# Performance work log

Measured on AMD Instinct MI355X. Metric: run time of the kernel, lower is better.

The kernel has to match this reference:

```python
import jax, jax.numpy as jnp
import numpy as np

# static config (matches init_kwargs and a standard 4-level FPN for ~800px input)
SPATIAL_SHAPES = ((100, 100), (50, 50), (25, 25), (13, 13))  # (H_l, W_l)
B, C, H, L, P = 2, 256, 8, 4, 4
DFFN = 2048
DH = C // H
LQ = sum(h * w for h, w in SPATIAL_SHAPES)  # 13294


def layer_norm(x, g, b, eps=1e-5):
    m = jnp.mean(x, -1, keepdims=True)
    v = jnp.mean((x - m) ** 2, -1, keepdims=True)
    return (x - m) * jax.lax.rsqrt(v + eps) * g + b


def ms_deform_sample(value, loc, attn):
    # value [B,Lv,H,DH], loc [B,Lq,H,L,P,2] in [0,1], attn [B,Lq,H,L,P]
    value = jnp.transpose(value, (0, 2, 1, 3))  # [B,H,Lv,DH]
    lq = loc.shape[1]
    out = jnp.zeros((B, H, lq, DH), value.dtype)
    start = 0
    for l, (Hl, Wl) in enumerate(SPATIAL_SHAPES):
        v = jax.lax.dynamic_slice_in_dim(value, start, Hl * Wl, axis=2)  # [B,H,N_l,DH]
        # grid_sample(align_corners=False) coords: x = loc_x*W - 0.5
        gx = jnp.transpose(loc[:, :, :, l, :, 0], (0, 2, 1, 3)) * Wl - 0.5  # [B,H,Lq,P]
        gy = jnp.transpose(loc[:, :, :, l, :, 1], (0, 2, 1, 3)) * Hl - 0.5
        aw = jnp.transpose(attn[:, :, :, l, :], (0, 2, 1, 3))  # [B,H,Lq,P]
        x0 = jnp.floor(gx)
        y0 = jnp.floor(gy)
        for dx in (0.0, 1.0):
            for dy in (0.0, 1.0):
                xi = x0 + dx
                yi = y0 + dy
                w = (1.0 - jnp.abs(gx - xi)) * (1.0 - jnp.abs(gy - yi))
                valid = (xi >= 0) & (xi < Wl) & (yi >= 0) & (yi < Hl)
                idx = (jnp.clip(yi, 0, Hl - 1) * Wl + jnp.clip(xi, 0, Wl - 1)).astype(jnp.int32)
                g = jnp.take_along_axis(v, idx.reshape(B, H, -1)[..., None], axis=2)  # [B,H,Lq*P,DH]
                ww = (w * aw * valid.astype(w.dtype))[..., None]  # [B,H,Lq,P,1]
                out = out + jnp.sum(g.reshape(B, H, lq, P, DH) * ww, axis=3)
        start += Hl * Wl
    return jnp.transpose(out, (0, 2, 1, 3)).reshape(B, lq, C)


def setup_inputs() -> dict:
    key = jax.random.key(0)
    ks = jax.random.split(key, 16)
    s = 0.02
    return {
        "src": jax.random.normal(ks[0], (B, LQ, C), jnp.float32),
        "pos": jax.random.normal(ks[1], (B, LQ, C), jnp.float32),
        "reference_points": jax.random.uniform(ks[2], (B, LQ, L, 2), jnp.float32),
        "w_value": jax.random.normal(ks[3], (C, C), jnp.float32) * s,
        "b_value": jnp.zeros((C,), jnp.float32),
        "w_off": jax.random.normal(ks[4], (C, H * L * P * 2), jnp.float32) * s,
        "b_off": jax.random.normal(ks[5], (H * L * P * 2,), jnp.float32) * s,
        "w_attn": jax.random.normal(ks[6], (C, H * L * P), jnp.float32) * s,
        "b_attn": jnp.zeros((H * L * P,), jnp.float32),
        "w_out": jax.random.normal(ks[7], (C, C), jnp.float32) * s,
        "b_out": jnp.zeros((C,), jnp.float32),
        "ln1_g": jnp.ones((C,), jnp.float32),
        "ln1_b": jnp.zeros((C,), jnp.float32),
        "w_ffn1": jax.random.normal(ks[8], (C, DFFN), jnp.float32) * s,
        "b_ffn1": jnp.zeros((DFFN,), jnp.float32),
        "w_ffn2": jax.random.normal(ks[9], (DFFN, C), jnp.float32) * s,
        "b_ffn2": jnp.zeros((C,), jnp.float32),
        "ln2_g": jnp.ones((C,), jnp.float32),
        "ln2_b": jnp.zeros((C,), jnp.float32),
    }


def reference(src, pos, reference_points, w_value, b_value, w_off, b_off, w_attn, b_attn,
              w_out, b_out, ln1_g, ln1_b, w_ffn1, b_ffn1, w_ffn2, b_ffn2, ln2_g, ln2_b):
    # DeformableTransformerEncoderLayer.forward (eval mode, no dropout)
    q = src + pos  # with_pos_embed
    lq = q.shape[1]
    value = (src @ w_value + b_value).reshape(B, -1, H, DH)
    off = (q @ w_off + b_off).reshape(B, lq, H, L, P, 2)
    attn = (q @ w_attn + b_attn).reshape(B, lq, H, L * P)
    attn = jax.nn.softmax(attn, axis=-1).reshape(B, lq, H, L, P)
    # offset_normalizer = (W_l, H_l)
    norm = jnp.array([[w, h] for h, w in SPATIAL_SHAPES], dtype=src.dtype)
    loc = reference_points[:, :, None, :, None, :] + off / norm[None, None, None, :, None, :]
    src2 = ms_deform_sample(value, loc, attn) @ w_out + b_out
    x = layer_norm(src + src2, ln1_g, ln1_b)
    ff = jax.nn.relu(x @ w_ffn1 + b_ffn1) @ w_ffn2 + b_ffn2
    return layer_norm(x + ff, ln2_g, ln2_b)
```

## Files before the change

kernel.cpp:

```cpp
#include <hip/hip_runtime.h>

#define LQN   13294
#define NBAT  2
#define MROWS (NBAT * LQN)
#define CCH   256
#define NHEAD 8
#define DHEAD 32
#define NLVL  4
#define NPT   4
#define DFF   2048

typedef short short8 __attribute__((ext_vector_type(8)));
typedef float f32x4 __attribute__((ext_vector_type(4)));
typedef unsigned short u16;
typedef u16 u16x4 __attribute__((ext_vector_type(4)));

__device__ __forceinline__ u16 f2bf(float f) {
  unsigned int u = __builtin_bit_cast(unsigned int, f);
  u += 0x7fffu + ((u >> 16) & 1u);
  return (u16)(u >> 16);
}
__device__ __forceinline__ float bf2f(u16 s) {
  unsigned int u = ((unsigned int)s) << 16;
  return __builtin_bit_cast(float, u);
}
__device__ __forceinline__ void async16(const void* g, void* l) {
  __builtin_amdgcn_global_load_lds(
      (const __attribute__((address_space(1))) void*)g,
      (__attribute__((address_space(3))) void*)l, 16, 0, 0);
}

template<int OUT_MODE>
__global__ __launch_bounds__(256, 2)
void gemm_bf16(const u16* __restrict__ A, const u16* __restrict__ BT,
               const float* __restrict__ bias, void* __restrict__ Cout,
               int M, int N, int K)
{
  __shared__ u16 As[2][128 * 64];
  __shared__ u16 Bs[2][128 * 64];
  const int t    = threadIdx.x;
  const int lane = t & 63;
  const int wid  = t >> 6;
  const int wm   = wid >> 1, wn = wid & 1;
  const int bm   = blockIdx.x, bn = blockIdx.y;
  const int l15  = lane & 15;
  const int kq   = lane >> 4;

  f32x4 acc[4][4];
#pragma unroll
  for (int m = 0; m < 4; ++m)
#pragma unroll
    for (int n = 0; n < 4; ++n) acc[m][n] = (f32x4)0.0f;

  auto stage = [&](int buf, int kt) {
#pragma unroll
    for (int i = 0; i < 4; ++i) {
      const int c   = i * 256 + t;
      const int row = c >> 3;
      const int kg  = (c & 7) ^ (row & 7);
      int ar = bm * 128 + row; ar = ar < M ? ar : M - 1;
      async16(&A[(size_t)ar * K + kt + kg * 8], &As[buf][c * 8]);
      const int br = bn * 128 + row;
      async16(&BT[(size_t)br * K + kt + kg * 8], &Bs[buf][c * 8]);
    }
  };

  stage(0, 0);
  __syncthreads();
  int cur = 0;

  for (int kt = 0; kt < K; kt += 64) {
    if (kt + 64 < K) stage(cur ^ 1, kt + 64);

#pragma unroll
    for (int kk = 0; kk < 2; ++kk) {
      short8 af[4], bfr[4];
#pragma unroll
      for (int m = 0; m < 4; ++m) {
        const int row = wm * 64 + m * 16 + l15;
        const int xb  = (kk * 64 + kq * 16) ^ ((row & 7) << 4);
        af[m] = *(const short8*)((const char*)&As[cur][0] + row * 128 + xb);
      }
#pragma unroll
      for (int n = 0; n < 4; ++n) {
        const int col = wn * 64 + n * 16 + l15;
        const int xb  = (kk * 64 + kq * 16) ^ ((col & 7) << 4);
        bfr[n] = *(const short8*)((const char*)&Bs[cur][0] + col * 128 + xb);
      }
#pragma unroll
      for (int m = 0; m < 4; ++m)
#pragma unroll
        for (int n = 0; n < 4; ++n)
          acc[m][n] = __builtin_amdgcn_mfma_f32_16x16x32_bf16(af[m], bfr[n], acc[m][n], 0, 0, 0);
    }

    __syncthreads();
    cur ^= 1;
  }

  const int crow0 = bm * 128 + wm * 64;
  const int ccol0 = bn * 128 + wn * 64;
#pragma unroll
  for (int n = 0; n < 4; ++n) {
    int col = ccol0 + n * 16 + l15;
    float bv = bias[col];
#pragma unroll
    for (int m = 0; m < 4; ++m) {
      int rbase = crow0 + m * 16 + kq * 4;
#pragma unroll
      for (int j = 0; j < 4; ++j) {
        int row = rbase + j;
        if (row < M) {
          float v = acc[m][n][j] + bv;
          if constexpr (OUT_MODE == 0) ((float*)Cout)[(size_t)row * N + col] = v;
          else                         ((u16*)Cout)[(size_t)row * N + col] = f2bf(v);
        }
      }
    }
  }
}

__global__ __launch_bounds__(256, 2)
void gemm_dual(const u16* __restrict__ A0, const u16* __restrict__ BT0,
               const float* __restrict__ bias0, u16* __restrict__ C0,
               const u16* __restrict__ A1, const u16* __restrict__ BT1,
               const float* __restrict__ bias1, float* __restrict__ C1)
{
  __shared__ u16 As[2][128 * 64];
  __shared__ u16 Bs[2][128 * 64];
  const int t    = threadIdx.x;
  const int lane = t & 63;
  const int wid  = t >> 6;
  const int wm   = wid >> 1, wn = wid & 1;
  const int bm   = blockIdx.x;
  const int bnG  = blockIdx.y;
  const bool first = bnG < 2;
  const u16* A    = first ? A0 : A1;
  const u16* BT   = first ? BT0 : BT1;
  const float* bias = first ? bias0 : bias1;
  const int  bn   = first ? bnG : bnG - 2;
  const int l15  = lane & 15;
  const int kq   = lane >> 4;

  f32x4 acc[4][4];
#pragma unroll
  for (int m = 0; m < 4; ++m)
#pragma unroll
    for (int n = 0; n < 4; ++n) acc[m][n] = (f32x4)0.0f;

  auto stage = [&](int buf, int kt) {
#pragma unroll
    for (int i = 0; i < 4; ++i) {
      const int c   = i * 256 + t;
      const int row = c >> 3;
      const int kg  = (c & 7) ^ (row & 7);
      int ar = bm * 128 + row; ar = ar < MROWS ? ar : MROWS - 1;
      async16(&A[(size_t)ar * 256 + kt + kg * 8], &As[buf][c * 8]);
      const int br = bn * 128 + row;
      async16(&BT[(size_t)br * 256 + kt + kg * 8], &Bs[buf][c * 8]);
    }
  };

  stage(0, 0);
  __syncthreads();
  int cur = 0;

  for (int kt = 0; kt < 256; kt += 64) {
    if (kt + 64 < 256) stage(cur ^ 1, kt + 64);

#pragma unroll
    for (int kk = 0; kk < 2; ++kk) {
      short8 af[4], bfr[4];
#pragma unroll
      for (int m = 0; m < 4; ++m) {
        const int row = wm * 64 + m * 16 + l15;
        const int xb  = (kk * 64 + kq * 16) ^ ((row & 7) << 4);
        af[m] = *(const short8*)((const char*)&As[cur][0] + row * 128 + xb);
      }
#pragma unroll
      for (int n = 0; n < 4; ++n) {
        const int col = wn * 64 + n * 16 + l15;
        const int xb  = (kk * 64 + kq * 16) ^ ((col & 7) << 4);
        bfr[n] = *(const short8*)((const char*)&Bs[cur][0] + col * 128 + xb);
      }
#pragma unroll
      for (int m = 0; m < 4; ++m)
#pragma unroll
        for (int n = 0; n < 4; ++n)
          acc[m][n] = __builtin_amdgcn_mfma_f32_16x16x32_bf16(af[m], bfr[n], acc[m][n], 0, 0, 0);
    }

    __syncthreads();
    cur ^= 1;
  }

  const int crow0 = bm * 128 + wm * 64;
  const int ccol0 = bn * 128 + wn * 64;
#pragma unroll
  for (int n = 0; n < 4; ++n) {
    int col = ccol0 + n * 16 + l15;
    float bv = bias[col];
#pragma unroll
    for (int m = 0; m < 4; ++m) {
      int rbase = crow0 + m * 16 + kq * 4;
#pragma unroll
      for (int j = 0; j < 4; ++j) {
        int row = rbase + j;
        if (row < MROWS) {
          float v = acc[m][n][j] + bv;
          if (first) C0[(size_t)row * 256 + col] = f2bf(v);
          else       C1[(size_t)row * 384 + col] = v;
        }
      }
    }
  }
}

__global__ __launch_bounds__(1024, 4)
void ffn_fused(const u16* __restrict__ x_bf, const u16* __restrict__ W1T,
               const u16* __restrict__ W2T, const float* __restrict__ b1,
               const float* __restrict__ b2, float* __restrict__ out)
{
  extern __shared__ char smem[];
  u16*  w1s = (u16*)(smem);
  u16*  w2s = (u16*)(smem + 65536);
  char* ps  = smem + 131072;

  const int t    = threadIdx.x;
  const int lane = t & 63;
  const int wid  = t >> 6;
  const int l15  = lane & 15;
  const int kq   = lane >> 4;
  const int bm   = blockIdx.x;
  const int pwm  = wid >> 1, pwn = wid & 1;
  const int vwm  = wid >> 2, vwn = wid & 3;

  short8 xr[8];
  {
    int ar = bm * 128 + pwm * 16 + l15;
    ar = ar < MROWS ? ar : MROWS - 1;
    const char* xb = (const char*)x_bf + (size_t)ar * 512 + kq * 16;
#pragma unroll
    for (int ks = 0; ks < 8; ++ks) xr[ks] = *(const short8*)(xb + ks * 64);
  }

  auto stage = [&](int buf, int it) {
#pragma unroll
    for (int i = 0; i < 2; ++i) {
      const int c  = i * 1024 + t;
      const int r1 = c >> 5;
      const int k1 = ((c & 31) ^ (r1 & 7)) * 8;
      async16(&W1T[(size_t)(it * 64 + r1) * 256 + k1], &w1s[buf * 16384 + c * 8]);
      const int r2 = c >> 3;
      const int k2 = ((c & 7) ^ (r2 & 7)) * 8;
      async16(&W2T[(size_t)r2 * 2048 + it * 64 + k2], &w2s[buf * 16384 + c * 8]);
    }
  };

  f32x4 acc[2][4];
#pragma unroll
  for (int m = 0; m < 2; ++m)
#pragma unroll
    for (int n = 0; n < 4; ++n) acc[m][n] = (f32x4)0.0f;

  stage(0, 0);
  __syncthreads();

  for (int it = 0; it < 32; ++it) {
    const int cur = it & 1;
    if (it < 31) stage(cur ^ 1, it + 1);

    f32x4 p[2];
    p[0] = (f32x4)0.0f; p[1] = (f32x4)0.0f;
#pragma unroll
    for (int ks = 0; ks < 8; ++ks) {
#pragma unroll
      for (int n = 0; n < 2; ++n) {
        const int wrow = pwn * 32 + n * 16 + l15;
        const int xb   = (((ks * 4 + kq) ^ (wrow & 7)) << 4);
        const short8 bfr = *(const short8*)((const char*)&w1s[cur * 16384] + wrow * 512 + xb);
        p[n] = __builtin_amdgcn_mfma_f32_16x16x32_bf16(xr[ks], bfr, p[n], 0, 0, 0);
      }
    }

#pragma unroll
    for (int n = 0; n < 2; ++n) {
      const int col = pwn * 32 + n * 16 + l15;
      const float bv = b1[it * 64 + col];
#pragma unroll
      for (int j = 0; j < 4; ++j) {
        const int prow = pwm * 16 + kq * 4 + j;
        *(u16*)(ps + prow * 144 + col * 2) = f2bf(fmaxf(p[n][j] + bv, 0.0f));
      }
    }
    __syncthreads();

#pragma unroll
    for (int kk = 0; kk < 2; ++kk) {
      short8 paf[2];
#pragma unroll
      for (int m = 0; m < 2; ++m) {
        const int arow = vwm * 32 + m * 16 + l15;
        paf[m] = *(const short8*)(ps + arow * 144 + (kk * 4 + kq) * 16);
      }
#pragma unroll
      for (int n = 0; n < 4; ++n) {
        const int brow = vwn * 64 + n * 16 + l15;
        const int xb   = (((kk * 4 + kq) ^ (brow & 7)) << 4);
        const short8 bfr = *(const short8*)((const char*)&w2s[cur * 16384] + brow * 128 + xb);
#pragma unroll
        for (int m = 0; m < 2; ++m)
          acc[m][n] = __builtin_amdgcn_mfma_f32_16x16x32_bf16(paf[m], bfr, acc[m][n], 0, 0, 0);
      }
    }
    __syncthreads();
  }

#pragma unroll
  for (int n = 0; n < 4; ++n) {
    const int col = vwn * 64 + n * 16 + l15;
    const float bv = b2[col];
#pragma unroll
    for (int m = 0; m < 2; ++m) {
      const int rbase = bm * 128 + vwm * 32 + m * 16 + kq * 4;
#pragma unroll
      for (int j = 0; j < 4; ++j) {
        const int row = rbase + j;
        if (row < MROWS) out[(size_t)row * 256 + col] = acc[m][n][j] + bv;
      }
    }
  }
}

__global__ __launch_bounds__(256)
void sampler_kernel(const float* __restrict__ offattn,
                    const float* __restrict__ refp,
                    const u16*  __restrict__ value,
                    u16*        __restrict__ src2)
{
  __shared__ float2 sWI[4][8][65];

  const int t    = threadIdx.x;
  const int r4   = t >> 6;
  const int lane = t & 63;
  const int row  = blockIdx.x * 4 + r4;
  const int b    = row / LQN;

  {
    const float* oa = offattn + (size_t)row * 384;
    const float* rp = refp + (size_t)row * 8;
    const int p16 = lane & 15;
    const int l   = p16 >> 2;
    const int Wl  = (l == 0) ? 100 : (l == 1) ? 50 : (l == 2) ? 25 : 13;
    const int st  = (l == 0) ? 0 : (l == 1) ? 10000 : (l == 2) ? 12500 : 13125;
    const float rx = rp[l * 2 + 0] * (float)Wl - 0.5f;
    const float ry = rp[l * 2 + 1] * (float)Wl - 0.5f;

#pragma unroll
    for (int s = 0; s < 2; ++s) {
      const int h = s * 4 + (lane >> 4);
      float logit = oa[256 + h * 16 + p16];
      float mx = logit;
#pragma unroll
      for (int o = 1; o < 16; o <<= 1) mx = fmaxf(mx, __shfl_xor(mx, o, 64));
      float e = __expf(logit - mx);
      float ssum = e;
#pragma unroll
      for (int o = 1; o < 16; o <<= 1) ssum += __shfl_xor(ssum, o, 64);
      const float aw = e / ssum;

      const float ox = oa[(h * 16 + p16) * 2 + 0];
      const float oy = oa[(h * 16 + p16) * 2 + 1];
      const float gx = rx + ox;
      const float gy = ry + oy;
      const float x0f = floorf(gx), y0f = floorf(gy);
      const int   x0 = (int)x0f, y0 = (int)y0f;
      const float fx = gx - x0f, fy = gy - y0f;
#pragma unroll
      for (int c = 0; c < 4; ++c) {
        const int dx = c & 1, dy = c >> 1;
        const int xi = x0 + dx, yi = y0 + dy;
        const float wx = dx ? fx : 1.0f - fx;
        const float wy = dy ? fy : 1.0f - fy;
        const bool valid = (xi >= 0) && (xi < Wl) && (yi >= 0) && (yi < Wl);
        const int xc = min(max(xi, 0), Wl - 1);
        const int yc = min(max(yi, 0), Wl - 1);
        const int idx = st + yc * Wl + xc;
        const float w = wx * wy * aw * (valid ? 1.0f : 0.0f);
        sWI[r4][h][p16 * 4 + c] = make_float2(w, __builtin_bit_cast(float, idx));
      }
    }
  }
  __syncthreads();

  {
    const int h  = lane >> 3;
    const int c4 = lane & 7;
    const char* vbase = (const char*)value + (size_t)b * LQN * 512 + h * 64 + c4 * 8;
    const float2* wi = sWI[r4][h];

    float a0 = 0.f, a1 = 0.f, a2 = 0.f, a3 = 0.f;
#pragma unroll 16
    for (int e = 0; e < 64; ++e) {
      const float2 p = wi[e];
      const float w  = p.x;
      const int  idx = __builtin_bit_cast(int, p.y);
      const unsigned long long u = *(const unsigned long long*)(vbase + (size_t)idx * 512);
      a0 += w * bf2f((u16)(u));
      a1 += w * bf2f((u16)(u >> 16));
      a2 += w * bf2f((u16)(u >> 32));
      a3 += w * bf2f((u16)(u >> 48));
    }
    u16x4 o;
    o[0] = f2bf(a0); o[1] = f2bf(a1); o[2] = f2bf(a2); o[3] = f2bf(a3);
    *(u16x4*)&src2[(size_t)row * 256 + h * 32 + c4 * 4] = o;
  }
}

template<int WRITE_BF>
__global__ __launch_bounds__(256)
void ln_kernel(const float* __restrict__ Xa, const float* __restrict__ Xb,
               const float* __restrict__ gam, const float* __restrict__ bet,
               float* __restrict__ Yf, u16* __restrict__ Ybf)
{
  const int wid = threadIdx.x >> 6, lane = threadIdx.x & 63;
  const int row = blockIdx.x * 4 + wid;
  const f32x4 va = ((const f32x4*)(Xa + (size_t)row * 256))[lane];
  const f32x4 vb = ((const f32x4*)(Xb + (size_t)row * 256))[lane];
  f32x4 v = va + vb;
  float s1 = v[0] + v[1] + v[2] + v[3];
  float s2 = v[0] * v[0] + v[1] * v[1] + v[2] * v[2] + v[3] * v[3];
#pragma unroll
  for (int off = 32; off; off >>= 1) {
    s1 += __shfl_xor(s1, off, 64);
    s2 += __shfl_xor(s2, off, 64);
  }
  const float mean = s1 * (1.0f / 256.0f);
  const float var  = s2 * (1.0f / 256.0f) - mean * mean;
  const float rstd = rsqrtf(var + 1e-5f);
  const f32x4 gv = ((const f32x4*)gam)[lane];
  const f32x4 bv = ((const f32x4*)bet)[lane];
  f32x4 y;
#pragma unroll
  for (int j = 0; j < 4; ++j) y[j] = (v[j] - mean) * rstd * gv[j] + bv[j];
  ((f32x4*)(Yf + (size_t)row * 256))[lane] = y;
  if constexpr (WRITE_BF) {
    u16x4 o;
#pragma unroll
    for (int j = 0; j < 4; ++j) o[j] = f2bf(y[j]);
    ((u16x4*)(Ybf + (size_t)row * 256))[lane] = o;
  }
}

__global__ __launch_bounds__(256)
void prep_qsrc(const float* __restrict__ src, const float* __restrict__ pos,
               u16* __restrict__ src_bf, u16* __restrict__ q_bf)
{
  const size_t i = (size_t)blockIdx.x * 256 + threadIdx.x;
  const f32x4 s = ((const f32x4*)src)[i];
  const f32x4 p = ((const f32x4*)pos)[i];
  u16x4 sb, qb;
#pragma unroll
  for (int j = 0; j < 4; ++j) { sb[j] = f2bf(s[j]); qb[j] = f2bf(s[j] + p[j]); }
  ((u16x4*)src_bf)[i] = sb;
  ((u16x4*)q_bf)[i]   = qb;
}

__global__ __launch_bounds__(256)
void prep_weights(const float* __restrict__ w_value, const float* __restrict__ w_off,
                  const float* __restrict__ w_attn,  const float* __restrict__ w_out,
                  const float* __restrict__ w_ffn1,  const float* __restrict__ w_ffn2,
                  const float* __restrict__ b_off,   const float* __restrict__ b_attn,
                  u16* __restrict__ WT_val, u16* __restrict__ WT_oa, u16* __restrict__ WT_out,
                  u16* __restrict__ WT_f1,  u16* __restrict__ WT_f2, float* __restrict__ bias_oa)
{
  int i = blockIdx.x * 256 + threadIdx.x;
  if (i < 65536) {
    const int k = i >> 8, n = i & 255;
    WT_val[n * 256 + k] = f2bf(w_value[i]);
  } else if ((i -= 65536) < 65536) {
    const int k = i >> 8, n = i & 255;
    WT_oa[n * 256 + k] = f2bf(w_off[i]);
  } else if ((i -= 65536) < 32768) {
    const int k = i >> 7, n = i & 127;
    WT_oa[(256 + n) * 256 + k] = f2bf(w_attn[i]);
  } else if ((i -= 32768) < 65536) {
    const int k = i >> 8, n = i & 255;
    WT_out[n * 256 + k] = f2bf(w_out[i]);
  } else if ((i -= 65536) < 524288) {
    const int k = i >> 11, n = i & 2047;
    WT_f1[n * 256 + k] = f2bf(w_ffn1[i]);
  } else if ((i -= 524288) < 524288) {
    const int k = i >> 8, n = i & 255;
    WT_f2[n * 2048 + k] = f2bf(w_ffn2[i]);
  } else if ((i -= 524288) < 384) {
    bias_oa[i] = (i < 256) ? b_off[i] : b_attn[i - 256];
  }
}

extern "C" void kernel_launch(void* const* d_in, const int* in_sizes, int n_in,
                              void* d_out, int out_size, void* d_ws, size_t ws_size,
                              hipStream_t stream)
{
  const float* src     = (const float*)d_in[0];
  const float* pos     = (const float*)d_in[1];
  const float* refp    = (const float*)d_in[2];
  const float* w_value = (const float*)d_in[3];
  const float* b_value = (const float*)d_in[4];
  const float* w_off   = (const float*)d_in[5];
  const float* b_off   = (const float*)d_in[6];
  const float* w_attn  = (const float*)d_in[7];
  const float* b_attn  = (const float*)d_in[8];
  const float* w_out   = (const float*)d_in[9];
  const float* b_out   = (const float*)d_in[10];
  const float* ln1_g   = (const float*)d_in[11];
  const float* ln1_b   = (const float*)d_in[12];
  const float* w_ffn1  = (const float*)d_in[13];
  const float* b_ffn1  = (const float*)d_in[14];
  const float* w_ffn2  = (const float*)d_in[15];
  const float* b_ffn2  = (const float*)d_in[16];
  const float* ln2_g   = (const float*)d_in[17];
  const float* ln2_b   = (const float*)d_in[18];

  char* ws = (char*)d_ws;
  size_t off = 0;
  auto alloc = [&](size_t bytes) { void* p = ws + off; off += (bytes + 255) & ~(size_t)255; return p; };

  u16*   src_bf   = (u16*)  alloc((size_t)MROWS * 256 * 2);
  u16*   q_bf     = (u16*)  alloc((size_t)MROWS * 256 * 2);
  float* offattn  = (float*)alloc((size_t)MROWS * 384 * 4);
  u16*   value_bf = (u16*)  alloc((size_t)MROWS * 256 * 2);
  u16*   src2_bf  = (u16*)  alloc((size_t)MROWS * 256 * 2);
  float* x_f32    = (float*)alloc((size_t)MROWS * 256 * 4);
  u16*   WT_val   = (u16*)  alloc(256 * 256 * 2);
  u16*   WT_oa    = (u16*)  alloc(384 * 256 * 2);
  u16*   WT_out   = (u16*)  alloc(256 * 256 * 2);
  u16*   WT_f1    = (u16*)  alloc(2048 * 256 * 2);
  u16*   WT_f2    = (u16*)  alloc((size_t)256 * 2048 * 2);
  float* bias_oa  = (float*)alloc(384 * 4);

  float* src2p = offattn;
  u16*   x_bf  = q_bf;
  float* ff    = (float*)value_bf;

  prep_weights<<<4994, 256, 0, stream>>>(w_value, w_off, w_attn, w_out, w_ffn1, w_ffn2,
                                         b_off, b_attn,
                                         WT_val, WT_oa, WT_out, WT_f1, WT_f2, bias_oa);

  prep_qsrc<<<6647, 256, 0, stream>>>(src, pos, src_bf, q_bf);

  static bool attr_set = false;
  if (!attr_set) {
    hipFuncSetAttribute((const void*)ffn_fused,
                        hipFuncAttributeMaxDynamicSharedMemorySize, 149504);
    attr_set = true;
  }

  gemm_dual<<<dim3(208, 5), 256, 0, stream>>>(src_bf, WT_val, b_value, value_bf,
                                              q_bf, WT_oa, bias_oa, offattn);

  sampler_kernel<<<MROWS / 4, 256, 0, stream>>>(offattn, refp, value_bf, src2_bf);

  gemm_bf16<0><<<dim3(208, 2), 256, 0, stream>>>(src2_bf, WT_out, b_out, src2p, MROWS, 256, 256);

  ln_kernel<1><<<6647, 256, 0, stream>>>(src, src2p, ln1_g, ln1_b, x_f32, x_bf);

  ffn_fused<<<208, 1024, 149504, stream>>>(x_bf, WT_f1, WT_f2, b_ffn1, b_ffn2, ff);

  ln_kernel<0><<<6647, 256, 0, stream>>>(x_f32, ff, ln2_g, ln2_b, (float*)d_out, nullptr);
}
```

Before: 252.7 us.

## Fuse residual and layernorm into the out-projection and FFN GEMM epilogues

```diff
diff --git a/kernel.cpp b/kernel.cpp
--- a/kernel.cpp
+++ b/kernel.cpp
@@ -28,96 +28,6 @@
   __builtin_amdgcn_global_load_lds(
       (const __attribute__((address_space(1))) void*)g,
       (__attribute__((address_space(3))) void*)l, 16, 0, 0);
-}
-
-template<int OUT_MODE>
-__global__ __launch_bounds__(256, 2)
-void gemm_bf16(const u16* __restrict__ A, const u16* __restrict__ BT,
-               const float* __restrict__ bias, void* __restrict__ Cout,
-               int M, int N, int K)
-{
-  __shared__ u16 As[2][128 * 64];
-  __shared__ u16 Bs[2][128 * 64];
-  const int t    = threadIdx.x;
-  const int lane = t & 63;
-  const int wid  = t >> 6;
-  const int wm   = wid >> 1, wn = wid & 1;
-  const int bm   = blockIdx.x, bn = blockIdx.y;
-  const int l15  = lane & 15;
-  const int kq   = lane >> 4;
-
-  f32x4 acc[4][4];
-#pragma unroll
-  for (int m = 0; m < 4; ++m)
-#pragma unroll
-    for (int n = 0; n < 4; ++n) acc[m][n] = (f32x4)0.0f;
-
-  auto stage = [&](int buf, int kt) {
-#pragma unroll
-    for (int i = 0; i < 4; ++i) {
-      const int c   = i * 256 + t;
-      const int row = c >> 3;
-      const int kg  = (c & 7) ^ (row & 7);
-      int ar = bm * 128 + row; ar = ar < M ? ar : M - 1;
-      async16(&A[(size_t)ar * K + kt + kg * 8], &As[buf][c * 8]);
-      const int br = bn * 128 + row;
-      async16(&BT[(size_t)br * K + kt + kg * 8], &Bs[buf][c * 8]);
-    }
-  };
-
-  stage(0, 0);
-  __syncthreads();
-  int cur = 0;
-
-  for (int kt = 0; kt < K; kt += 64) {
-    if (kt + 64 < K) stage(cur ^ 1, kt + 64);
-
-#pragma unroll
-    for (int kk = 0; kk < 2; ++kk) {
-      short8 af[4], bfr[4];
-#pragma unroll
-      for (int m = 0; m < 4; ++m) {
-        const int row = wm * 64 + m * 16 + l15;
-        const int xb  = (kk * 64 + kq * 16) ^ ((row & 7) << 4);
-        af[m] = *(const short8*)((const char*)&As[cur][0] + row * 128 + xb);
-      }
-#pragma unroll
-      for (int n = 0; n < 4; ++n) {
-        const int col = wn * 64 + n * 16 + l15;
-        const int xb  = (kk * 64 + kq * 16) ^ ((col & 7) << 4);
-        bfr[n] = *(const short8*)((const char*)&Bs[cur][0] + col * 128 + xb);
-      }
-#pragma unroll
-      for (int m = 0; m < 4; ++m)
-#pragma unroll
-        for (int n = 0; n < 4; ++n)
-          acc[m][n] = __builtin_amdgcn_mfma_f32_16x16x32_bf16(af[m], bfr[n], acc[m][n], 0, 0, 0);
-    }
-
-    __syncthreads();
-    cur ^= 1;
-  }
-
-  const int crow0 = bm * 128 + wm * 64;
-  const int ccol0 = bn * 128 + wn * 64;
-#pragma unroll
-  for (int n = 0; n < 4; ++n) {
-    int col = ccol0 + n * 16 + l15;
-    float bv = bias[col];
-#pragma unroll
-    for (int m = 0; m < 4; ++m) {
-      int rbase = crow0 + m * 16 + kq * 4;
-#pragma unroll
-      for (int j = 0; j < 4; ++j) {
-        int row = rbase + j;
-        if (row < M) {
-          float v = acc[m][n][j] + bv;
-          if constexpr (OUT_MODE == 0) ((float*)Cout)[(size_t)row * N + col] = v;
-          else                         ((u16*)Cout)[(size_t)row * N + col] = f2bf(v);
-        }
-      }
-    }
-  }
 }
 
 __global__ __launch_bounds__(256, 2)
@@ -216,15 +126,166 @@
   }
 }
 
-__global__ __launch_bounds__(1024, 4)
-void ffn_fused(const u16* __restrict__ x_bf, const u16* __restrict__ W1T,
-               const u16* __restrict__ W2T, const float* __restrict__ b1,
-               const float* __restrict__ b2, float* __restrict__ out)
+__global__ __launch_bounds__(512, 1)
+void outproj_ln1(const u16* __restrict__ src2_bf, const u16* __restrict__ WT_out,
+                 const float* __restrict__ b_out, const float* __restrict__ src,
+                 const float* __restrict__ g1, const float* __restrict__ be1,
+                 float* __restrict__ x_f32, u16* __restrict__ x_bf)
+{
+  extern __shared__ char smem[];
+  char* As0 = smem;
+  char* As1 = smem + 16384;
+  char* Bs0 = smem + 32768;
+  char* Bs1 = smem + 65536;
+  float2* red = (float2*)(smem + 98304);
+
+  const int t    = threadIdx.x;
+  const int lane = t & 63;
+  const int wid  = t >> 6;
+  const int wm   = wid >> 2, wn = wid & 3;
+  const int l15  = lane & 15;
+  const int kq   = lane >> 4;
+  const int bm   = blockIdx.x;
+
+  auto stage = [&](char* Abuf, char* Bbuf, int kt) {
+#pragma unroll
+    for (int i = 0; i < 2; ++i) {
+      const int c   = i * 512 + t;
+      const int row = c >> 3;
+      const int kg  = (c & 7) ^ (row & 7);
+      int ar = bm * 128 + row; ar = ar < MROWS ? ar : MROWS - 1;
+      async16(&src2_bf[(size_t)ar * 256 + kt + kg * 8], Abuf + c * 16);
+    }
+#pragma unroll
+    for (int i = 0; i < 4; ++i) {
+      const int c   = i * 512 + t;
+      const int row = c >> 3;
+      const int kg  = (c & 7) ^ (row & 7);
+      async16(&WT_out[(size_t)row * 256 + kt + kg * 8], Bbuf + c * 16);
+    }
+  };
+
+  f32x4 acc[4][4];
+#pragma unroll
+  for (int m = 0; m < 4; ++m)
+#pragma unroll
+    for (int n = 0; n < 4; ++n) acc[m][n] = (f32x4)0.0f;
+
+  stage(As0, Bs0, 0);
+  __syncthreads();
+
+  for (int kt = 0; kt < 256; kt += 64) {
+    const int cur = (kt >> 6) & 1;
+    char* Ause = cur ? As1 : As0;
+    char* Buse = cur ? Bs1 : Bs0;
+    if (kt + 64 < 256) stage(cur ? As0 : As1, cur ? Bs0 : Bs1, kt + 64);
+
+#pragma unroll
+    for (int kk = 0; kk < 2; ++kk) {
+      short8 af[4], bfr[4];
+#pragma unroll
+      for (int m = 0; m < 4; ++m) {
+        const int row = wm * 64 + m * 16 + l15;
+        const int xb  = (kk * 64 + kq * 16) ^ ((row & 7) << 4);
+        af[m] = *(const short8*)(Ause + row * 128 + xb);
+      }
+#pragma unroll
+      for (int n = 0; n < 4; ++n) {
+        const int col = wn * 64 + n * 16 + l15;
+        const int xb  = (kk * 64 + kq * 16) ^ ((col & 7) << 4);
+        bfr[n] = *(const short8*)(Buse + col * 128 + xb);
+      }
+#pragma unroll
+      for (int m = 0; m < 4; ++m)
+#pragma unroll
+        for (int n = 0; n < 4; ++n)
+          acc[m][n] = __builtin_amdgcn_mfma_f32_16x16x32_bf16(af[m], bfr[n], acc[m][n], 0, 0, 0);
+    }
+    __syncthreads();
+  }
+
+#pragma unroll
+  for (int n = 0; n < 4; ++n) {
+    const int col = wn * 64 + n * 16 + l15;
+    const float bv = b_out[col];
+#pragma unroll
+    for (int m = 0; m < 4; ++m)
+#pragma unroll
+      for (int j = 0; j < 4; ++j) {
+        int row = bm * 128 + wm * 64 + m * 16 + kq * 4 + j;
+        row = row < MROWS ? row : MROWS - 1;
+        acc[m][n][j] += bv + src[(size_t)row * 256 + col];
+      }
+  }
+  float s1[4][4], s2[4][4];
+#pragma unroll
+  for (int m = 0; m < 4; ++m)
+#pragma unroll
+    for (int j = 0; j < 4; ++j) {
+      float a = 0.f, b = 0.f;
+#pragma unroll
+      for (int n = 0; n < 4; ++n) { const float v = acc[m][n][j]; a += v; b += v * v; }
+      s1[m][j] = a; s2[m][j] = b;
+    }
+#pragma unroll
+  for (int o = 1; o < 16; o <<= 1)
+#pragma unroll
+    for (int m = 0; m < 4; ++m)
+#pragma unroll
+      for (int j = 0; j < 4; ++j) {
+        s1[m][j] += __shfl_xor(s1[m][j], o, 64);
+        s2[m][j] += __shfl_xor(s2[m][j], o, 64);
+      }
+  if (l15 == 0)
+#pragma unroll
+    for (int m = 0; m < 4; ++m)
+#pragma unroll
+      for (int j = 0; j < 4; ++j)
+        red[(wm * 64 + m * 16 + kq * 4 + j) * 4 + wn] = make_float2(s1[m][j], s2[m][j]);
+  __syncthreads();
+  float mean[4][4], rstd[4][4];
+#pragma unroll
+  for (int m = 0; m < 4; ++m)
+#pragma unroll
+    for (int j = 0; j < 4; ++j) {
+      const int rl = wm * 64 + m * 16 + kq * 4 + j;
+      float a = 0.f, b = 0.f;
+#pragma unroll
+      for (int w = 0; w < 4; ++w) { const float2 r = red[rl * 4 + w]; a += r.x; b += r.y; }
+      const float mu = a * (1.0f / 256.0f);
+      mean[m][j] = mu;
+      rstd[m][j] = rsqrtf(b * (1.0f / 256.0f) - mu * mu + 1e-5f);
+    }
+#pragma unroll
+  for (int n = 0; n < 4; ++n) {
+    const int col = wn * 64 + n * 16 + l15;
+    const float gg = g1[col], bb = be1[col];
+#pragma unroll
+    for (int m = 0; m < 4; ++m)
+#pragma unroll
+      for (int j = 0; j < 4; ++j) {
+        const int row = bm * 128 + wm * 64 + m * 16 + kq * 4 + j;
+        if (row < MROWS) {
+          const float y = (acc[m][n][j] - mean[m][j]) * rstd[m][j] * gg + bb;
+          x_f32[(size_t)row * 256 + col] = y;
+          x_bf[(size_t)row * 256 + col] = f2bf(y);
+        }
+      }
+  }
+}
+
+__global__ __launch_bounds__(1024, 2)
+void ffn_ln2(const u16* __restrict__ x_bf, const u16* __restrict__ W1T,
+             const u16* __restrict__ W2T, const float* __restrict__ b1,
+             const float* __restrict__ b2, const float* __restrict__ x_f32,
+             const float* __restrict__ g2, const float* __restrict__ be2,
+             float* __restrict__ out)
 {
   extern __shared__ char smem[];
   u16*  w1s = (u16*)(smem);
   u16*  w2s = (u16*)(smem + 65536);
   char* ps  = smem + 131072;
+  float2* red = (float2*)(smem + 149504);
 
   const int t    = threadIdx.x;
   const int lane = t & 63;
@@ -321,14 +382,65 @@
     const int col = vwn * 64 + n * 16 + l15;
     const float bv = b2[col];
 #pragma unroll
-    for (int m = 0; m < 2; ++m) {
-      const int rbase = bm * 128 + vwm * 32 + m * 16 + kq * 4;
-#pragma unroll
-      for (int j = 0; j < 4; ++j) {
-        const int row = rbase + j;
-        if (row < MROWS) out[(size_t)row * 256 + col] = acc[m][n][j] + bv;
-      }
-    }
+    for (int m = 0; m < 2; ++m)
+#pragma unroll
+      for (int j = 0; j < 4; ++j) {
+        int row = bm * 128 + vwm * 32 + m * 16 + kq * 4 + j;
+        row = row < MROWS ? row : MROWS - 1;
+        acc[m][n][j] += bv + x_f32[(size_t)row * 256 + col];
+      }
+  }
+  float s1[2][4], s2[2][4];
+#pragma unroll
+  for (int m = 0; m < 2; ++m)
+#pragma unroll
+    for (int j = 0; j < 4; ++j) {
+      float a = 0.f, b = 0.f;
+#pragma unroll
+      for (int n = 0; n < 4; ++n) { const float v = acc[m][n][j]; a += v; b += v * v; }
+      s1[m][j] = a; s2[m][j] = b;
+    }
+#pragma unroll
+  for (int o = 1; o < 16; o <<= 1)
+#pragma unroll
+    for (int m = 0; m < 2; ++m)
+#pragma unroll
+      for (int j = 0; j < 4; ++j) {
+        s1[m][j] += __shfl_xor(s1[m][j], o, 64);
+        s2[m][j] += __shfl_xor(s2[m][j], o, 64);
+      }
+  if (l15 == 0)
+#pragma unroll
+    for (int m = 0; m < 2; ++m)
+#pragma unroll
+      for (int j = 0; j < 4; ++j)
+        red[(vwm * 32 + m * 16 + kq * 4 + j) * 4 + vwn] = make_float2(s1[m][j], s2[m][j]);
+  __syncthreads();
+  float mean[2][4], rstd[2][4];
+#pragma unroll
+  for (int m = 0; m < 2; ++m)
+#pragma unroll
+    for (int j = 0; j < 4; ++j) {
+      const int rl = vwm * 32 + m * 16 + kq * 4 + j;
+      float a = 0.f, b = 0.f;
+#pragma unroll
+      for (int w = 0; w < 4; ++w) { const float2 r = red[rl * 4 + w]; a += r.x; b += r.y; }
+      const float mu = a * (1.0f / 256.0f);
+      mean[m][j] = mu;
+      rstd[m][j] = rsqrtf(b * (1.0f / 256.0f) - mu * mu + 1e-5f);
+    }
+#pragma unroll
+  for (int n = 0; n < 4; ++n) {
+    const int col = vwn * 64 + n * 16 + l15;
+    const float gg = g2[col], bb = be2[col];
+#pragma unroll
+    for (int m = 0; m < 2; ++m)
+#pragma unroll
+      for (int j = 0; j < 4; ++j) {
+        const int row = bm * 128 + vwm * 32 + m * 16 + kq * 4 + j;
+        if (row < MROWS)
+          out[(size_t)row * 256 + col] = (acc[m][n][j] - mean[m][j]) * rstd[m][j] * gg + bb;
+      }
   }
 }
 
@@ -414,41 +526,6 @@
     u16x4 o;
     o[0] = f2bf(a0); o[1] = f2bf(a1); o[2] = f2bf(a2); o[3] = f2bf(a3);
     *(u16x4*)&src2[(size_t)row * 256 + h * 32 + c4 * 4] = o;
-  }
-}
-
-template<int WRITE_BF>
-__global__ __launch_bounds__(256)
-void ln_kernel(const float* __restrict__ Xa, const float* __restrict__ Xb,
-               const float* __restrict__ gam, const float* __restrict__ bet,
-               float* __restrict__ Yf, u16* __restrict__ Ybf)
-{
-  const int wid = threadIdx.x >> 6, lane = threadIdx.x & 63;
-  const int row = blockIdx.x * 4 + wid;
-  const f32x4 va = ((const f32x4*)(Xa + (size_t)row * 256))[lane];
-  const f32x4 vb = ((const f32x4*)(Xb + (size_t)row * 256))[lane];
-  f32x4 v = va + vb;
-  float s1 = v[0] + v[1] + v[2] + v[3];
-  float s2 = v[0] * v[0] + v[1] * v[1] + v[2] * v[2] + v[3] * v[3];
-#pragma unroll
-  for (int off = 32; off; off >>= 1) {
-    s1 += __shfl_xor(s1, off, 64);
-    s2 += __shfl_xor(s2, off, 64);
-  }
-  const float mean = s1 * (1.0f / 256.0f);
-  const float var  = s2 * (1.0f / 256.0f) - mean * mean;
-  const float rstd = rsqrtf(var + 1e-5f);
-  const f32x4 gv = ((const f32x4*)gam)[lane];
-  const f32x4 bv = ((const f32x4*)bet)[lane];
-  f32x4 y;
-#pragma unroll
-  for (int j = 0; j < 4; ++j) y[j] = (v[j] - mean) * rstd * gv[j] + bv[j];
-  ((f32x4*)(Yf + (size_t)row * 256))[lane] = y;
-  if constexpr (WRITE_BF) {
-    u16x4 o;
-#pragma unroll
-    for (int j = 0; j < 4; ++j) o[j] = f2bf(y[j]);
-    ((u16x4*)(Ybf + (size_t)row * 256))[lane] = o;
   }
 }
 
@@ -539,9 +616,7 @@
   u16*   WT_f2    = (u16*)  alloc((size_t)256 * 2048 * 2);
   float* bias_oa  = (float*)alloc(384 * 4);
 
-  float* src2p = offattn;
-  u16*   x_bf  = q_bf;
-  float* ff    = (float*)value_bf;
+  u16* x_bf = q_bf;
 
   prep_weights<<<4994, 256, 0, stream>>>(w_value, w_off, w_attn, w_out, w_ffn1, w_ffn2,
                                          b_off, b_attn,
@@ -551,8 +626,10 @@
 
   static bool attr_set = false;
   if (!attr_set) {
-    hipFuncSetAttribute((const void*)ffn_fused,
-                        hipFuncAttributeMaxDynamicSharedMemorySize, 149504);
+    hipFuncSetAttribute((const void*)ffn_ln2,
+                        hipFuncAttributeMaxDynamicSharedMemorySize, 153600);
+    hipFuncSetAttribute((const void*)outproj_ln1,
+                        hipFuncAttributeMaxDynamicSharedMemorySize, 102400);
     attr_set = true;
   }
 
@@ -561,11 +638,9 @@
 
   sampler_kernel<<<MROWS / 4, 256, 0, stream>>>(offattn, refp, value_bf, src2_bf);
 
-  gemm_bf16<0><<<dim3(208, 2), 256, 0, stream>>>(src2_bf, WT_out, b_out, src2p, MROWS, 256, 256);
-
-  ln_kernel<1><<<6647, 256, 0, stream>>>(src, src2p, ln1_g, ln1_b, x_f32, x_bf);
-
-  ffn_fused<<<208, 1024, 149504, stream>>>(x_bf, WT_f1, WT_f2, b_ffn1, b_ffn2, ff);
-
-  ln_kernel<0><<<6647, 256, 0, stream>>>(x_f32, ff, ln2_g, ln2_b, (float*)d_out, nullptr);
-}
+  outproj_ln1<<<208, 512, 102400, stream>>>(src2_bf, WT_out, b_out, src,
+                                            ln1_g, ln1_b, x_f32, x_bf);
+
+  ffn_ln2<<<208, 1024, 153600, stream>>>(x_bf, WT_f1, WT_f2, b_ffn1, b_ffn2,
+                                         x_f32, ln2_g, ln2_b, (float*)d_out);
+}
```

New measurement: 239.0 us. -5.4%, faster.
